# Performance work log

Hardware: AMD Instinct MI355X
Metric: run time of the kernel (lower is better)

Reference implementation:

```python
import jax, jax.numpy as jnp
import numpy as np

N_NODES = 50000
N_EDGES = 800000
MAX_ITER = 20  # torchdeq default f_max_iter=40; fixed iteration count for a tractable jit-able baseline
K = 3          # TAGConv default number of hops
INS, EMB, HID, OUT = 4, 64, 128, 1


def setup_inputs():
    key = jax.random.key(0)
    ks = jax.random.split(key, 12)
    def lin(k, fan_in, fan_out):
        return jax.random.normal(k, (fan_in, fan_out), jnp.float32) / np.sqrt(fan_in)
    def tag_w(k, fan_in, fan_out):
        # stacked weights for the K+1 TAGConv linear maps: [K+1, in, out]
        return jax.random.normal(k, (K + 1, fan_in, fan_out), jnp.float32) / np.sqrt(fan_in * (K + 1))
    return {
        "x": jax.random.normal(ks[0], (N_NODES, INS), jnp.float32),
        "pos": jax.random.normal(ks[1], (N_NODES, 3), jnp.float32),
        "edge_attr": jax.random.uniform(ks[2], (N_EDGES,), jnp.float32),
        "up_w1": lin(ks[3], INS, EMB), "up_b1": jnp.zeros((EMB,), jnp.float32),
        "up_w2": lin(ks[4], EMB, EMB), "up_b2": jnp.zeros((EMB,), jnp.float32),
        "c1_w": tag_w(ks[5], EMB + 3, HID), "c1_b": jnp.zeros((HID,), jnp.float32),
        "c2_w": tag_w(ks[6], HID, HID), "c2_b": jnp.zeros((HID,), jnp.float32),
        "c3_w": tag_w(ks[7], HID, EMB), "c3_b": jnp.zeros((EMB,), jnp.float32),
        "down_w1": lin(ks[8], EMB, OUT), "down_b1": jnp.zeros((OUT,), jnp.float32),
        "down_w2": lin(ks[9], OUT, OUT), "down_b2": jnp.zeros((OUT,), jnp.float32),
        "edge_index": jax.random.randint(ks[10], (2, N_EDGES), 0, N_NODES, jnp.int32),
    }


def _gcn_norm(row, col, edge_attr, n):
    # PyG gcn_norm with edge weights, no self loops (TAGConv default)
    deg = jax.ops.segment_sum(edge_attr, col, num_segments=n)
    safe = jnp.where(deg > 0, deg, 1.0)
    dinv = jnp.where(deg > 0, jax.lax.rsqrt(safe), 0.0)
    return dinv[row] * edge_attr * dinv[col]


def _mlp(x, w1, b1, w2, b2):
    # torch F.gelu default = exact erf gelu
    return jax.nn.gelu(x @ w1 + b1, approximate=False) @ w2 + b2


def reference(x, pos, edge_attr, up_w1, up_b1, up_w2, up_b2, c1_w, c1_b, c2_w, c2_b, c3_w, c3_b, down_w1, down_b1, down_w2, down_b2, edge_index):
    n = x.shape[0]
    row, col = edge_index[0], edge_index[1]
    norm = _gcn_norm(row, col, edge_attr, n)

    def tag(h, W, b):
        # TAGConv: sum_k lin_k( A_hat^k x ) + bias
        out = h @ W[0]
        for k in range(1, W.shape[0]):
            h = jax.ops.segment_sum(h[row] * norm[:, None], col, num_segments=n)  # [E,C] gather-scatter
            out = out + h @ W[k]
        return out + b

    def gnn(z):
        h = jnp.concatenate([z, pos], axis=1)
        h = jax.nn.relu(tag(h, c1_w, c1_b))
        h = jax.nn.relu(tag(h, c2_w, c2_b))  # F.dropout is identity in eval mode
        h = tag(h, c3_w, c3_b)
        return jax.nn.log_softmax(h, axis=1)

    z0 = _mlp(x, up_w1, up_b1, up_w2, up_b2)
    z = jax.lax.fori_loop(0, MAX_ITER, lambda i, zz: gnn(zz), z0)  # fixed-point solver
    z_star = gnn(z)  # phantom-gradient step (torchdeq grad=1)
    out = _mlp(z_star, down_w1, down_b1, down_w2, down_b2)
    return out, z_star
```

## Files before the change

### kernel.cpp

```cpp
#include <hip/hip_runtime.h>
#include <hip/hip_bf16.h>

#define N_NODES 50000
#define N_EDGES 800000
#define MAX_ITER 20

typedef __attribute__((ext_vector_type(8))) short bf16x8;
typedef __attribute__((ext_vector_type(4))) float f32x4;
typedef __attribute__((ext_vector_type(2))) float f32x2;
typedef unsigned char uchar;

__device__ __forceinline__ float gelu_f(float x){
  return 0.5f*x*(1.0f+erff(x*0.70710678118654752f));
}
__device__ __forceinline__ ushort f2b(float f){
  uint x = __float_as_uint(f);
  uint r = (x + 0x7fffu + ((x>>16)&1u)) >> 16;
  return (ushort)r;
}

#if __has_builtin(__builtin_amdgcn_cvt_pk_f32_fp8) && __has_builtin(__builtin_amdgcn_cvt_pk_fp8_f32)
#define HW_FP8 1
#endif

__device__ __forceinline__ uint fp8_enc1_sw(float x){
  uint u = __float_as_uint(x);
  uint s = (u>>24)&0x80u;
  int e = (int)((u>>23)&0xffu);
  uint m = u&0x7fffffu;
  uint m3 = (m + 0x80000u)>>20;
  if (m3==8u){ e+=1; m3=0u; }
  int e8 = e-120;
  if (e8<=0) return s;
  if (e8>=15) return s|0x7eu;
  return s | ((uint)e8<<3) | m3;
}
__device__ __forceinline__ float fp8_dec1_sw(uint b){
  uint s=(b&0x80u)<<24;
  uint em=b&0x7fu;
  if (em==0u) return __uint_as_float(s);
  if ((em>>3)==0u) return (s?-1.f:1.f)*(float)em*0.001953125f;
  return __uint_as_float(s | ((em+960u)<<20));
}
__device__ __forceinline__ void fp8_dec8(uint lo, uint hi, float* d){
#ifdef HW_FP8
  f32x2 a = __builtin_amdgcn_cvt_pk_f32_fp8(lo,false);
  f32x2 b = __builtin_amdgcn_cvt_pk_f32_fp8(lo,true);
  f32x2 c = __builtin_amdgcn_cvt_pk_f32_fp8(hi,false);
  f32x2 e = __builtin_amdgcn_cvt_pk_f32_fp8(hi,true);
  d[0]=a[0];d[1]=a[1];d[2]=b[0];d[3]=b[1];d[4]=c[0];d[5]=c[1];d[6]=e[0];d[7]=e[1];
#else
  d[0]=fp8_dec1_sw(lo&0xffu);        d[1]=fp8_dec1_sw((lo>>8)&0xffu);
  d[2]=fp8_dec1_sw((lo>>16)&0xffu);  d[3]=fp8_dec1_sw(lo>>24);
  d[4]=fp8_dec1_sw(hi&0xffu);        d[5]=fp8_dec1_sw((hi>>8)&0xffu);
  d[6]=fp8_dec1_sw((hi>>16)&0xffu);  d[7]=fp8_dec1_sw(hi>>24);
#endif
}
__device__ __forceinline__ uint fp8_enc4(float a,float b,float c,float d){
#ifdef HW_FP8
  uint u = __builtin_amdgcn_cvt_pk_fp8_f32(a,b,0u,false);
  u = __builtin_amdgcn_cvt_pk_fp8_f32(c,d,u,true);
  return u;
#else
  return fp8_enc1_sw(a) | (fp8_enc1_sw(b)<<8) | (fp8_enc1_sw(c)<<16) | (fp8_enc1_sw(d)<<24);
#endif
}
__device__ __forceinline__ uchar fp8_enc1(float a){
#ifdef HW_FP8
  return (uchar)(__builtin_amdgcn_cvt_pk_fp8_f32(a,a,0u,false)&0xffu);
#else
  return (uchar)fp8_enc1_sw(a);
#endif
}

__global__ void deg_cnt_kernel(const int* __restrict__ col, const float* __restrict__ attr,
                               float* __restrict__ deg, int* __restrict__ cnt){
  int e = blockIdx.x*256 + threadIdx.x;
  if (e < N_EDGES){
    int c = col[e];
    atomicAdd(&deg[c], attr[e]);
    atomicAdd(&cnt[c], 1);
  }
}

__global__ void norm_kernel(const int* __restrict__ row, const int* __restrict__ col,
                            const float* __restrict__ attr, const float* __restrict__ deg,
                            float* __restrict__ nrm){
  int e = blockIdx.x*256 + threadIdx.x;
  if (e < N_EDGES){
    float dr = deg[row[e]], dc = deg[col[e]];
    float ir = dr > 0.f ? rsqrtf(dr) : 0.f;
    float ic = dc > 0.f ? rsqrtf(dc) : 0.f;
    nrm[e] = ir * attr[e] * ic;
  }
}

__global__ void scan_kernel(const int* __restrict__ cnt, int* __restrict__ starts,
                            int* __restrict__ cursor){
  __shared__ int buf[1024];
  __shared__ int carry;
  int tid = threadIdx.x;
  if (tid==0) carry = 0;
  __syncthreads();
  for (int base=0; base<N_NODES; base+=1024){
    int i = base+tid;
    int v = (i<N_NODES)? cnt[i] : 0;
    int cv = carry;
    buf[tid]=v;
    __syncthreads();
    for (int off=1; off<1024; off<<=1){
      int t = (tid>=off)? buf[tid-off] : 0;
      __syncthreads();
      buf[tid]+=t;
      __syncthreads();
    }
    int excl = buf[tid]-v+cv;
    if (i<N_NODES){ starts[i]=excl; cursor[i]=excl; }
    __syncthreads();
    if (tid==0) carry = cv + buf[1023];
    __syncthreads();
  }
  if (tid==0) starts[N_NODES] = carry;
}

__global__ void fill_kernel(const int* __restrict__ row, const int* __restrict__ col,
                            const float* __restrict__ nrm, int* __restrict__ cursor,
                            int* __restrict__ csr_row, float* __restrict__ csr_nrm){
  int e = blockIdx.x*256+threadIdx.x;
  if (e<N_EDGES){
    int c = col[e];
    int p = atomicAdd(&cursor[c],1);
    csr_row[p]=row[e];
    csr_nrm[p]=nrm[e];
  }
}

__global__ void pack_w1(const float* __restrict__ W, ushort* __restrict__ PB){
  int i = blockIdx.x*256+threadIdx.x;
  if (i < 4*8*128*8){
    int e = i&7; int n = (i>>3)&127; int kb = (i>>10)&7; int j = i>>13;
    int k = kb*8+e;
    PB[i] = f2b(W[((size_t)j*67 + k)*128 + n]);
  }
}
__global__ void pack_w2(const float* __restrict__ W, ushort* __restrict__ PB){
  int i = blockIdx.x*256+threadIdx.x;
  if (i < 4*16*128*8){
    int e = i&7; int n = (i>>3)&127; int kb = (i>>10)&15; int j = i>>14;
    int k = kb*8+e;
    PB[i] = f2b(W[((size_t)j*128 + k)*128 + n]);
  }
}
__global__ void pack_w3(const float* __restrict__ W, ushort* __restrict__ PB){
  int i = blockIdx.x*256+threadIdx.x;
  if (i < 16*256*8){
    int e = i&7; int n = (i>>3)&255; int kb = i>>11;
    int k = kb*8+e;
    PB[i] = f2b(W[(((size_t)(n>>6))*128 + k)*64 + (n&63)]);
  }
}

__global__ __launch_bounds__(256) void mlp_up_kernel(
    const float* __restrict__ x, const float* __restrict__ w1, const float* __restrict__ b1,
    const float* __restrict__ w2, const float* __restrict__ b2,
    ushort* __restrict__ z, uchar* __restrict__ z8){
  __shared__ float sw1[4*64];
  __shared__ float sw2[64*64];
  __shared__ float sb1[64], sb2[64];
  __shared__ float t1s[4][64];
  int tid = threadIdx.x;
  for (int i=tid;i<256;i+=256) sw1[i]=w1[i];
  for (int i=tid;i<4096;i+=256) sw2[i]=w2[i];
  if (tid<64){ sb1[tid]=b1[tid]; sb2[tid]=b2[tid]; }
  __syncthreads();
  int g = tid>>6;
  int c = tid&63;
  int node = blockIdx.x*4 + g;
  float acc = sb1[c];
  #pragma unroll
  for (int k=0;k<4;k++) acc += x[node*4+k]*sw1[k*64+c];
  t1s[g][c] = gelu_f(acc);
  __syncthreads();
  float acc2 = sb2[c];
  #pragma unroll 8
  for (int k=0;k<64;k++) acc2 += t1s[g][k]*sw2[k*64+c];
  z[(size_t)node*64+c] = f2b(acc2);
  z8[(size_t)node*64+c] = fp8_enc1(acc2);
}

template<int LDIN>
__global__ void posprop(const float* __restrict__ in, float* __restrict__ out,
                        const int* __restrict__ starts, const int* __restrict__ crow,
                        const float* __restrict__ cnrm){
  int v = blockIdx.x*256+threadIdx.x;
  if (v >= N_NODES) return;
  int s=starts[v], e=starts[v+1];
  float a0=0.f,a1=0.f,a2=0.f;
  for (int i=s;i<e;++i){
    int r=crow[i]; float nm=cnrm[i];
    a0 = fmaf(in[(size_t)r*LDIN+0], nm, a0);
    a1 = fmaf(in[(size_t)r*LDIN+1], nm, a1);
    a2 = fmaf(in[(size_t)r*LDIN+2], nm, a2);
  }
  float4 o = {a0,a1,a2,0.f};
  *(float4*)(out + (size_t)v*4) = o;
}

__global__ __launch_bounds__(256) void posbias_kernel(
    const float* __restrict__ pos, const float* __restrict__ P1,
    const float* __restrict__ P2, const float* __restrict__ P3,
    const float* __restrict__ c1w, const float* __restrict__ c1b,
    ushort* __restrict__ pb){
  __shared__ float sw[4][3][128];
  int tid=threadIdx.x;
  for (int i=tid; i<4*3*128; i+=256){
    int cc=i&127; int d=(i>>7)%3; int j=i/(3*128);
    sw[j][d][cc] = c1w[((size_t)j*67 + 64 + d)*128 + cc];
  }
  __syncthreads();
  int idx = blockIdx.x*256+tid;
  if (idx < N_NODES*128){
    int n = idx>>7, cc = idx&127;
    float a = c1b[cc];
    #pragma unroll
    for (int d=0;d<3;d++) a = fmaf(pos[(size_t)n*3+d], sw[0][d][cc], a);
    #pragma unroll
    for (int d=0;d<3;d++) a = fmaf(P1[(size_t)n*4+d], sw[1][d][cc], a);
    #pragma unroll
    for (int d=0;d<3;d++) a = fmaf(P2[(size_t)n*4+d], sw[2][d][cc], a);
    #pragma unroll
    for (int d=0;d<3;d++) a = fmaf(P3[(size_t)n*4+d], sw[3][d][cc], a);
    pb[idx]=f2b(a);
  }
}

template<int MODE, bool IN8, bool OUT8>
__global__ __launch_bounds__(256) void prop64k(
    const void* __restrict__ hin, ushort* __restrict__ obf,
    uchar* __restrict__ of8, float* __restrict__ of32,
    const ushort* __restrict__ adj, const float* __restrict__ bias,
    const int* __restrict__ starts, const int* __restrict__ crow,
    const float* __restrict__ cnrm){
  constexpr bool WBF = (MODE==0) || (MODE==2) || (MODE==1 && !OUT8);
  int wv = threadIdx.x >> 6;
  int v = blockIdx.x*4 + wv;
  int t = threadIdx.x & 63;
  int g = t >> 3;
  int c = t & 7;
  int s = starts[v], e = starts[v+1];
  float acc[8] = {0,0,0,0,0,0,0,0};
  for (int i=s; i<e; i+=64){
    int cnt = e - i; if (cnt > 64) cnt = 64;
    int r = 0; float nm = 0.f;
    if (t < cnt){ r = crow[i+t]; nm = cnrm[i+t]; }
    for (int jb=0; jb<cnt; jb+=8){
      int rr = __shfl(r, jb+g, 64);
      float nmj = __shfl(nm, jb+g, 64);
      float hv[8];
      if (IN8){
        uint2 d = *(const uint2*)((const uchar*)hin + (size_t)rr*64 + c*8);
        fp8_dec8(d.x, d.y, hv);
      } else {
        uint4 d = *(const uint4*)((const ushort*)hin + (size_t)rr*64 + c*8);
        const uint* dp = (const uint*)&d;
        #pragma unroll
        for (int q=0;q<4;q++){
          hv[2*q]   = __uint_as_float(dp[q]<<16);
          hv[2*q+1] = __uint_as_float(dp[q]&0xffff0000u);
        }
      }
      #pragma unroll
      for (int q=0;q<8;q++) acc[q] = fmaf(hv[q], nmj, acc[q]);
    }
  }
  #pragma unroll
  for (int q=0;q<8;q++){
    acc[q] += __shfl_xor(acc[q], 8, 64);
    acc[q] += __shfl_xor(acc[q], 16, 64);
    acc[q] += __shfl_xor(acc[q], 32, 64);
  }
  if (MODE==0 || MODE==1){
    if (g==0){
      float val[8];
      if (MODE==1){
        uint4 av = *(const uint4*)(adj + (size_t)v*64 + c*8);
        const uint* ap=(const uint*)&av;
        #pragma unroll
        for (int q=0;q<4;q++){
          val[2*q]   = acc[2*q]   + __uint_as_float(ap[q]<<16);
          val[2*q+1] = acc[2*q+1] + __uint_as_float(ap[q]&0xffff0000u);
        }
      } else {
        #pragma unroll
        for (int q=0;q<8;q++) val[q]=acc[q];
      }
      if (WBF){
        uint4 o; uint* op=(uint*)&o;
        #pragma unroll
        for (int q=0;q<4;q++) op[q] = (uint)f2b(val[2*q]) | ((uint)f2b(val[2*q+1])<<16);
        *(uint4*)(obf + (size_t)v*64 + c*8) = o;
      }
      if (OUT8){
        uint2 o8;
        o8.x = fp8_enc4(val[0],val[1],val[2],val[3]);
        o8.y = fp8_enc4(val[4],val[5],val[6],val[7]);
        *(uint2*)(of8 + (size_t)v*64 + c*8) = o8;
      }
    }
  } else {
    uint4 av = *(const uint4*)(adj + (size_t)v*64 + c*8);
    const uint* ap=(const uint*)&av;
    float vv[8];
    #pragma unroll
    for (int q=0;q<4;q++){
      vv[2*q]   = acc[2*q]   + __uint_as_float(ap[q]<<16)         + bias[c*8+2*q];
      vv[2*q+1] = acc[2*q+1] + __uint_as_float(ap[q]&0xffff0000u) + bias[c*8+2*q+1];
    }
    float m = vv[0];
    #pragma unroll
    for (int q=1;q<8;q++) m = fmaxf(m, vv[q]);
    m = fmaxf(m, __shfl_xor(m,1,64));
    m = fmaxf(m, __shfl_xor(m,2,64));
    m = fmaxf(m, __shfl_xor(m,4,64));
    float ss = 0.f;
    #pragma unroll
    for (int q=0;q<8;q++) ss += __expf(vv[q]-m);
    ss += __shfl_xor(ss,1,64);
    ss += __shfl_xor(ss,2,64);
    ss += __shfl_xor(ss,4,64);
    float lse = m + __logf(ss);
    if (g==0){
      if (MODE==2){
        uint4 o; uint* op=(uint*)&o;
        #pragma unroll
        for (int q=0;q<4;q++) op[q] = (uint)f2b(vv[2*q]-lse) | ((uint)f2b(vv[2*q+1]-lse)<<16);
        *(uint4*)(obf + (size_t)v*64 + c*8) = o;
        if (OUT8){
          uint2 o8;
          o8.x = fp8_enc4(vv[0]-lse,vv[1]-lse,vv[2]-lse,vv[3]-lse);
          o8.y = fp8_enc4(vv[4]-lse,vv[5]-lse,vv[6]-lse,vv[7]-lse);
          *(uint2*)(of8 + (size_t)v*64 + c*8) = o8;
        }
      } else {
        float* zo = of32 + (size_t)v*64 + c*8;
        float4 o0 = {vv[0]-lse, vv[1]-lse, vv[2]-lse, vv[3]-lse};
        float4 o1 = {vv[4]-lse, vv[5]-lse, vv[6]-lse, vv[7]-lse};
        *(float4*)zo = o0;
        *(float4*)(zo+4) = o1;
      }
    }
  }
}

template<bool IN8, bool OUT8>
__global__ __launch_bounds__(256) void prop128k(
    const void* __restrict__ hin, ushort* __restrict__ obf,
    uchar* __restrict__ of8,
    const int* __restrict__ starts, const int* __restrict__ crow,
    const float* __restrict__ cnrm){
  int wv = threadIdx.x >> 6;
  int v = blockIdx.x*4 + wv;
  int t = threadIdx.x & 63;
  int g = t >> 4;
  int c = t & 15;
  int s = starts[v], e = starts[v+1];
  float acc[8] = {0,0,0,0,0,0,0,0};
  for (int i=s; i<e; i+=64){
    int cnt = e - i; if (cnt > 64) cnt = 64;
    int r = 0; float nm = 0.f;
    if (t < cnt){ r = crow[i+t]; nm = cnrm[i+t]; }
    for (int jb=0; jb<cnt; jb+=4){
      int rr  = __shfl(r,  jb+g, 64);
      float nmj = __shfl(nm, jb+g, 64);
      float hv[8];
      if (IN8){
        uint2 d = *(const uint2*)((const uchar*)hin + (size_t)rr*128 + c*8);
        fp8_dec8(d.x, d.y, hv);
      } else {
        uint4 d = *(const uint4*)((const ushort*)hin + (size_t)rr*128 + c*8);
        const uint* dp = (const uint*)&d;
        #pragma unroll
        for (int q=0;q<4;q++){
          hv[2*q]   = __uint_as_float(dp[q]<<16);
          hv[2*q+1] = __uint_as_float(dp[q]&0xffff0000u);
        }
      }
      #pragma unroll
      for (int q=0;q<8;q++) acc[q] = fmaf(hv[q], nmj, acc[q]);
    }
  }
  #pragma unroll
  for (int q=0;q<8;q++){
    acc[q] += __shfl_xor(acc[q], 16, 64);
    acc[q] += __shfl_xor(acc[q], 32, 64);
  }
  if (g==0){
    uint4 o; uint* op=(uint*)&o;
    #pragma unroll
    for (int q=0;q<4;q++) op[q] = (uint)f2b(acc[2*q]) | ((uint)f2b(acc[2*q+1])<<16);
    *(uint4*)(obf + (size_t)v*128 + c*8) = o;
    if (OUT8){
      uint2 o8;
      o8.x = fp8_enc4(acc[0],acc[1],acc[2],acc[3]);
      o8.y = fp8_enc4(acc[4],acc[5],acc[6],acc[7]);
      *(uint2*)(of8 + (size_t)v*128 + c*8) = o8;
    }
  }
}

template<int KC, bool PERNODE_BIAS, bool OUT8>
__global__ __launch_bounds__(256) void gemm4in(
    const ushort* __restrict__ H0, const ushort* __restrict__ H1,
    const ushort* __restrict__ H2, const ushort* __restrict__ H3,
    const ushort* __restrict__ PB, const void* __restrict__ biasp,
    ushort* __restrict__ out, uchar* __restrict__ out8){
  constexpr int NT = 8;
  constexpr int NKS = KC/32;
  int lane = threadIdx.x & 63;
  int wv   = threadIdx.x >> 6;
  int m0 = blockIdx.x*64 + wv*16;
  int lr = lane & 15, lg = lane >> 4;
  int arow = m0 + lr; if (arow > N_NODES-1) arow = N_NODES-1;
  const ushort* Hs[4] = {H0,H1,H2,H3};
  f32x4 acc[NT];
  #pragma unroll
  for (int t=0;t<NT;t++) acc[t] = (f32x4){0.f,0.f,0.f,0.f};
  #pragma unroll
  for (int j=0;j<4;j++){
    const ushort* Hj  = Hs[j] + (size_t)arow*KC + lg*8;
    const ushort* PBj = PB + (size_t)j*(KC/8)*128*8;
    #pragma unroll
    for (int ks=0; ks<NKS; ks++){
      bf16x8 af = *(const bf16x8*)(Hj + ks*32);
      int kb = ks*4 + lg;
      #pragma unroll
      for (int t=0;t<NT;t++){
        bf16x8 bf = *(const bf16x8*)(PBj + ((size_t)kb*128 + t*16 + lr)*8);
        acc[t] = __builtin_amdgcn_mfma_f32_16x16x32_bf16(af, bf, acc[t], 0, 0, 0);
      }
    }
  }
  #pragma unroll
  for (int t=0;t<NT;t++){
    #pragma unroll
    for (int q=0;q<4;q++){
      int node = m0 + lg*4 + q;
      if (node < N_NODES){
        int col = t*16 + lr;
        float b;
        if (PERNODE_BIAS) b = __uint_as_float(((uint)((const ushort*)biasp)[(size_t)node*128+col])<<16);
        else              b = ((const float*)biasp)[col];
        float vo = fmaxf(acc[t][q] + b, 0.f);
        out[(size_t)node*128 + col] = f2b(vo);
        if (OUT8) out8[(size_t)node*128 + col] = fp8_enc1(vo);
      }
    }
  }
}

__global__ __launch_bounds__(256) void gemm_y(
    const ushort* __restrict__ T2, const ushort* __restrict__ PB,
    ushort* __restrict__ Y, uchar* __restrict__ Y3_8){
  constexpr int NT = 16;
  int lane = threadIdx.x & 63;
  int wv   = threadIdx.x >> 6;
  int m0 = blockIdx.x*64 + wv*16;
  int lr = lane & 15, lg = lane >> 4;
  int arow = m0 + lr; if (arow > N_NODES-1) arow = N_NODES-1;
  f32x4 acc[NT];
  #pragma unroll
  for (int t=0;t<NT;t++) acc[t] = (f32x4){0.f,0.f,0.f,0.f};
  const ushort* Hj = T2 + (size_t)arow*128 + lg*8;
  #pragma unroll
  for (int ks=0; ks<4; ks++){
    bf16x8 af = *(const bf16x8*)(Hj + ks*32);
    int kb = ks*4 + lg;
    #pragma unroll
    for (int t=0;t<NT;t++){
      bf16x8 bf = *(const bf16x8*)(PB + ((size_t)kb*256 + t*16 + lr)*8);
      acc[t] = __builtin_amdgcn_mfma_f32_16x16x32_bf16(af, bf, acc[t], 0, 0, 0);
    }
  }
  #pragma unroll
  for (int t=0;t<NT;t++){
    int n = t*16 + lr;
    int j = n >> 6, cc = n & 63;
    #pragma unroll
    for (int q=0;q<4;q++){
      int node = m0 + lg*4 + q;
      if (node < N_NODES){
        Y[(size_t)j*N_NODES*64 + (size_t)node*64 + cc] = f2b(acc[t][q]);
        if (j==3) Y3_8[(size_t)node*64 + cc] = fp8_enc1(acc[t][q]);
      }
    }
  }
}

__global__ __launch_bounds__(256) void mlp_down_kernel(
    const float* __restrict__ zs, const float* __restrict__ dw1, const float* __restrict__ db1,
    const float* __restrict__ dw2, const float* __restrict__ db2, float* __restrict__ out){
  int node = blockIdx.x*4 + (threadIdx.x>>6);
  int c = threadIdx.x & 63;
  float v = zs[(size_t)node*64+c]*dw1[c];
  #pragma unroll
  for (int off=32; off; off>>=1) v += __shfl_xor(v, off, 64);
  if (c==0) out[node] = gelu_f(v + db1[0]) * dw2[0] + db2[0];
}

extern "C" void kernel_launch(void* const* d_in, const int* in_sizes, int n_in,
                              void* d_out, int out_size, void* d_ws, size_t ws_size,
                              hipStream_t stream){
  const float* x     = (const float*)d_in[0];
  const float* pos   = (const float*)d_in[1];
  const float* eattr = (const float*)d_in[2];
  const float* up_w1 = (const float*)d_in[3];
  const float* up_b1 = (const float*)d_in[4];
  const float* up_w2 = (const float*)d_in[5];
  const float* up_b2 = (const float*)d_in[6];
  const float* c1_w  = (const float*)d_in[7];
  const float* c1_b  = (const float*)d_in[8];
  const float* c2_w  = (const float*)d_in[9];
  const float* c2_b  = (const float*)d_in[10];
  const float* c3_w  = (const float*)d_in[11];
  const float* c3_b  = (const float*)d_in[12];
  const float* dw1   = (const float*)d_in[13];
  const float* db1   = (const float*)d_in[14];
  const float* dw2   = (const float*)d_in[15];
  const float* db2   = (const float*)d_in[16];
  const int*   eidx  = (const int*)d_in[17];
  const int* row = eidx;
  const int* col = eidx + N_EDGES;

  char* wsp = (char*)d_ws;
  size_t off = 0;
  auto alloc = [&](size_t bytes)->char*{
    char* p = wsp + off;
    off = (off + bytes + 255) & ~(size_t)255;
    return p;
  };
  float*  deg    = (float*)alloc((size_t)N_NODES*4);
  int*    cnt    = (int*)  alloc((size_t)N_NODES*4);
  int*    starts = (int*)  alloc((size_t)(N_NODES+1)*4);
  int*    cursor = (int*)  alloc((size_t)N_NODES*4);
  float*  nrm    = (float*)alloc((size_t)N_EDGES*4);
  int*    crow   = (int*)  alloc((size_t)N_EDGES*4);
  float*  cnrm   = (float*)alloc((size_t)N_EDGES*4);
  float*  P1     = (float*)alloc((size_t)N_NODES*4*4);
  float*  P2     = (float*)alloc((size_t)N_NODES*4*4);
  float*  P3     = (float*)alloc((size_t)N_NODES*4*4);
  ushort* pbias  = (ushort*)alloc((size_t)N_NODES*128*2);
  ushort* z      = (ushort*)alloc((size_t)N_NODES*64*2);
  ushort* q1     = (ushort*)alloc((size_t)N_NODES*64*2);
  ushort* q2     = (ushort*)alloc((size_t)N_NODES*64*2);
  ushort* q3     = (ushort*)alloc((size_t)N_NODES*64*2);
  ushort* t1     = (ushort*)alloc((size_t)N_NODES*128*2);
  ushort* p1     = (ushort*)alloc((size_t)N_NODES*128*2);
  ushort* p2     = (ushort*)alloc((size_t)N_NODES*128*2);
  ushort* p3     = (ushort*)alloc((size_t)N_NODES*128*2);
  ushort* t2     = (ushort*)alloc((size_t)N_NODES*128*2);
  ushort* PB1    = (ushort*)alloc((size_t)4*8*128*8*2);
  ushort* PB2    = (ushort*)alloc((size_t)4*16*128*8*2);
  ushort* PB3    = (ushort*)alloc((size_t)16*256*8*2);
  uchar*  z8     = (uchar*)alloc((size_t)N_NODES*64);
  uchar*  q1_8   = (uchar*)alloc((size_t)N_NODES*64);
  uchar*  q2_8   = (uchar*)alloc((size_t)N_NODES*64);
  uchar*  t1_8   = (uchar*)alloc((size_t)N_NODES*128);
  uchar*  p1_8   = (uchar*)alloc((size_t)N_NODES*128);
  uchar*  p2_8   = (uchar*)alloc((size_t)N_NODES*128);
  uchar*  Y3_8   = (uchar*)alloc((size_t)N_NODES*64);
  uchar*  u1_8   = (uchar*)alloc((size_t)N_NODES*64);
  uchar*  u2_8   = (uchar*)alloc((size_t)N_NODES*64);

  ushort* Y  = p1;
  ushort* Y0 = Y;
  ushort* Y1 = Y + (size_t)1*N_NODES*64;
  ushort* Y2 = Y + (size_t)2*N_NODES*64;
  ushort* Y3 = Y + (size_t)3*N_NODES*64;
  ushort* u1 = q1;
  ushort* u2 = q2;

  float* outv  = (float*)d_out;
  float* zstar = (float*)d_out + N_NODES;

  hipMemsetAsync(deg, 0, (size_t)N_NODES*4, stream);
  hipMemsetAsync(cnt, 0, (size_t)N_NODES*4, stream);
  int eb = (N_EDGES+255)/256;
  deg_cnt_kernel<<<eb,256,0,stream>>>(col, eattr, deg, cnt);
  norm_kernel<<<eb,256,0,stream>>>(row, col, eattr, deg, nrm);
  scan_kernel<<<1,1024,0,stream>>>(cnt, starts, cursor);
  fill_kernel<<<eb,256,0,stream>>>(row, col, nrm, cursor, crow, cnrm);
  pack_w1<<<128,256,0,stream>>>(c1_w, PB1);
  pack_w2<<<256,256,0,stream>>>(c2_w, PB2);
  pack_w3<<<128,256,0,stream>>>(c3_w, PB3);
  mlp_up_kernel<<<N_NODES/4,256,0,stream>>>(x, up_w1, up_b1, up_w2, up_b2, z, z8);

  int nb = (N_NODES+255)/256;
  posprop<3><<<nb,256,0,stream>>>(pos, P1, starts, crow, cnrm);
  posprop<4><<<nb,256,0,stream>>>(P1,  P2, starts, crow, cnrm);
  posprop<4><<<nb,256,0,stream>>>(P2,  P3, starts, crow, cnrm);
  posbias_kernel<<<(N_NODES*128)/256,256,0,stream>>>(pos, P1, P2, P3, c1_w, c1_b, pbias);

  const int gprop = N_NODES/4;
  const int ggemm = (N_NODES+63)/64;

  for (int it=0; it<=MAX_ITER; ++it){
    if (it < MAX_ITER){
      prop64k<0,true,true> <<<gprop,256,0,stream>>>(z8,   q1, q1_8, nullptr, nullptr, nullptr, starts, crow, cnrm);
      prop64k<0,true,true> <<<gprop,256,0,stream>>>(q1_8, q2, q2_8, nullptr, nullptr, nullptr, starts, crow, cnrm);
      prop64k<0,true,false><<<gprop,256,0,stream>>>(q2_8, q3, nullptr, nullptr, nullptr, nullptr, starts, crow, cnrm);
      gemm4in<64,true,true><<<ggemm,256,0,stream>>>(z,q1,q2,q3,PB1,pbias,t1,t1_8);

      prop128k<true,true> <<<gprop,256,0,stream>>>(t1_8, p1, p1_8, starts, crow, cnrm);
      prop128k<true,true> <<<gprop,256,0,stream>>>(p1_8, p2, p2_8, starts, crow, cnrm);
      prop128k<true,false><<<gprop,256,0,stream>>>(p2_8, p3, nullptr, starts, crow, cnrm);
      gemm4in<128,false,false><<<ggemm,256,0,stream>>>(t1,p1,p2,p3,PB2,c2_b,t2,nullptr);

      gemm_y<<<ggemm,256,0,stream>>>(t2, PB3, Y, Y3_8);
      prop64k<1,true,true><<<gprop,256,0,stream>>>(Y3_8, nullptr, u1_8, nullptr, Y2, nullptr, starts, crow, cnrm);
      prop64k<1,true,true><<<gprop,256,0,stream>>>(u1_8, nullptr, u2_8, nullptr, Y1, nullptr, starts, crow, cnrm);
      prop64k<2,true,true><<<gprop,256,0,stream>>>(u2_8, z, z8, nullptr, Y0, c3_b, starts, crow, cnrm);
    } else {
      prop64k<0,false,false><<<gprop,256,0,stream>>>(z,  q1, nullptr, nullptr, nullptr, nullptr, starts, crow, cnrm);
      prop64k<0,false,false><<<gprop,256,0,stream>>>(q1, q2, nullptr, nullptr, nullptr, nullptr, starts, crow, cnrm);
      prop64k<0,false,false><<<gprop,256,0,stream>>>(q2, q3, nullptr, nullptr, nullptr, nullptr, starts, crow, cnrm);
      gemm4in<64,true,false><<<ggemm,256,0,stream>>>(z,q1,q2,q3,PB1,pbias,t1,nullptr);

      prop128k<false,false><<<gprop,256,0,stream>>>(t1, p1, nullptr, starts, crow, cnrm);
      prop128k<false,false><<<gprop,256,0,stream>>>(p1, p2, nullptr, starts, crow, cnrm);
      prop128k<false,false><<<gprop,256,0,stream>>>(p2, p3, nullptr, starts, crow, cnrm);
      gemm4in<128,false,false><<<ggemm,256,0,stream>>>(t1,p1,p2,p3,PB2,c2_b,t2,nullptr);

      gemm_y<<<ggemm,256,0,stream>>>(t2, PB3, Y, Y3_8);
      prop64k<1,false,false><<<gprop,256,0,stream>>>(Y3, u1, nullptr, nullptr, Y2, nullptr, starts, crow, cnrm);
      prop64k<1,false,false><<<gprop,256,0,stream>>>(u1, u2, nullptr, nullptr, Y1, nullptr, starts, crow, cnrm);
      prop64k<3,false,false><<<gprop,256,0,stream>>>(u2, nullptr, nullptr, zstar, Y0, c3_b, starts, crow, cnrm);
    }
  }
  mlp_down_kernel<<<N_NODES/4,256,0,stream>>>(zstar, dw1, db1, dw2, db2, outv);
}
```

Before: 6.940 ms.

## Split 128-channel fp8 propagation into two 64-channel halves for cache locality

Stores the fp8 copies of 128-wide hidden features as two separate 64-byte-per-node planes and adds a propagation kernel in which each block gathers only one half. Block indices are interleaved so neighbouring blocks alternate halves, which shrinks the working set each gather touches and is meant to raise L2/MALL hit rates on the random edge gathers. In exchange every edge index and norm is read twice, the per-node reduction needs an extra shuffle stage, and twice as many blocks are launched.

```diff
diff --git a/kernel.cpp b/kernel.cpp
--- a/kernel.cpp
+++ b/kernel.cpp
@@ -352,10 +352,60 @@
   }
 }
 
-template<bool IN8, bool OUT8>
+template<bool OUT8>
+__global__ __launch_bounds__(256) void prop128s(
+    const uchar* __restrict__ inlo, const uchar* __restrict__ inhi,
+    ushort* __restrict__ obf, uchar* __restrict__ o8lo, uchar* __restrict__ o8hi,
+    const int* __restrict__ starts, const int* __restrict__ crow,
+    const float* __restrict__ cnrm){
+  int xs   = blockIdx.x & 7;
+  int half = xs >> 2;
+  int sub  = (blockIdx.x >> 3)*4 + (xs & 3);
+  const uchar* hin = half ? inhi : inlo;
+  uchar* of8 = half ? o8hi : o8lo;
+  int wv = threadIdx.x >> 6;
+  int v = sub*4 + wv;
+  int t = threadIdx.x & 63;
+  int g = t >> 3;
+  int c = t & 7;
+  int s = starts[v], e = starts[v+1];
+  float acc[8] = {0,0,0,0,0,0,0,0};
+  for (int i=s; i<e; i+=64){
+    int cnt = e - i; if (cnt > 64) cnt = 64;
+    int r = 0; float nm = 0.f;
+    if (t < cnt){ r = crow[i+t]; nm = cnrm[i+t]; }
+    for (int jb=0; jb<cnt; jb+=8){
+      int rr = __shfl(r, jb+g, 64);
+      float nmj = __shfl(nm, jb+g, 64);
+      float hv[8];
+      uint2 d = *(const uint2*)(hin + (size_t)rr*64 + c*8);
+      fp8_dec8(d.x, d.y, hv);
+      #pragma unroll
+      for (int q=0;q<8;q++) acc[q] = fmaf(hv[q], nmj, acc[q]);
+    }
+  }
+  #pragma unroll
+  for (int q=0;q<8;q++){
+    acc[q] += __shfl_xor(acc[q], 8, 64);
+    acc[q] += __shfl_xor(acc[q], 16, 64);
+    acc[q] += __shfl_xor(acc[q], 32, 64);
+  }
+  if (g==0){
+    uint4 o; uint* op=(uint*)&o;
+    #pragma unroll
+    for (int q=0;q<4;q++) op[q] = (uint)f2b(acc[2*q]) | ((uint)f2b(acc[2*q+1])<<16);
+    *(uint4*)(obf + (size_t)v*128 + half*64 + c*8) = o;
+    if (OUT8){
+      uint2 o8;
+      o8.x = fp8_enc4(acc[0],acc[1],acc[2],acc[3]);
+      o8.y = fp8_enc4(acc[4],acc[5],acc[6],acc[7]);
+      *(uint2*)(of8 + (size_t)v*64 + c*8) = o8;
+    }
+  }
+}
+
 __global__ __launch_bounds__(256) void prop128k(
-    const void* __restrict__ hin, ushort* __restrict__ obf,
-    uchar* __restrict__ of8,
+    const ushort* __restrict__ hin, ushort* __restrict__ obf,
     const int* __restrict__ starts, const int* __restrict__ crow,
     const float* __restrict__ cnrm){
   int wv = threadIdx.x >> 6;
@@ -372,21 +422,13 @@
     for (int jb=0; jb<cnt; jb+=4){
       int rr  = __shfl(r,  jb+g, 64);
       float nmj = __shfl(nm, jb+g, 64);
-      float hv[8];
-      if (IN8){
-        uint2 d = *(const uint2*)((const uchar*)hin + (size_t)rr*128 + c*8);
-        fp8_dec8(d.x, d.y, hv);
-      } else {
-        uint4 d = *(const uint4*)((const ushort*)hin + (size_t)rr*128 + c*8);
-        const uint* dp = (const uint*)&d;
-        #pragma unroll
-        for (int q=0;q<4;q++){
-          hv[2*q]   = __uint_as_float(dp[q]<<16);
-          hv[2*q+1] = __uint_as_float(dp[q]&0xffff0000u);
-        }
-      }
+      uint4 d = *(const uint4*)(hin + (size_t)rr*128 + c*8);
+      const uint* dp = (const uint*)&d;
       #pragma unroll
-      for (int q=0;q<8;q++) acc[q] = fmaf(hv[q], nmj, acc[q]);
+      for (int q=0;q<4;q++){
+        acc[2*q]   = fmaf(__uint_as_float(dp[q]<<16),         nmj, acc[2*q]);
+        acc[2*q+1] = fmaf(__uint_as_float(dp[q]&0xffff0000u), nmj, acc[2*q+1]);
+      }
     }
   }
   #pragma unroll
@@ -399,12 +441,6 @@
     #pragma unroll
     for (int q=0;q<4;q++) op[q] = (uint)f2b(acc[2*q]) | ((uint)f2b(acc[2*q+1])<<16);
     *(uint4*)(obf + (size_t)v*128 + c*8) = o;
-    if (OUT8){
-      uint2 o8;
-      o8.x = fp8_enc4(acc[0],acc[1],acc[2],acc[3]);
-      o8.y = fp8_enc4(acc[4],acc[5],acc[6],acc[7]);
-      *(uint2*)(of8 + (size_t)v*128 + c*8) = o8;
-    }
   }
 }
 
@@ -413,7 +449,7 @@
     const ushort* __restrict__ H0, const ushort* __restrict__ H1,
     const ushort* __restrict__ H2, const ushort* __restrict__ H3,
     const ushort* __restrict__ PB, const void* __restrict__ biasp,
-    ushort* __restrict__ out, uchar* __restrict__ out8){
+    ushort* __restrict__ out, uchar* __restrict__ out8lo, uchar* __restrict__ out8hi){
   constexpr int NT = 8;
   constexpr int NKS = KC/32;
   int lane = threadIdx.x & 63;
@@ -452,7 +488,10 @@
         else              b = ((const float*)biasp)[col];
         float vo = fmaxf(acc[t][q] + b, 0.f);
         out[(size_t)node*128 + col] = f2b(vo);
-        if (OUT8) out8[(size_t)node*128 + col] = fp8_enc1(vo);
+        if (OUT8){
+          if (col < 64) out8lo[(size_t)node*64 + col]      = fp8_enc1(vo);
+          else          out8hi[(size_t)node*64 + col - 64] = fp8_enc1(vo);
+        }
       }
     }
   }
@@ -564,9 +603,12 @@
   uchar*  z8     = (uchar*)alloc((size_t)N_NODES*64);
   uchar*  q1_8   = (uchar*)alloc((size_t)N_NODES*64);
   uchar*  q2_8   = (uchar*)alloc((size_t)N_NODES*64);
-  uchar*  t1_8   = (uchar*)alloc((size_t)N_NODES*128);
-  uchar*  p1_8   = (uchar*)alloc((size_t)N_NODES*128);
-  uchar*  p2_8   = (uchar*)alloc((size_t)N_NODES*128);
+  uchar*  t1_8lo = (uchar*)alloc((size_t)N_NODES*64);
+  uchar*  t1_8hi = (uchar*)alloc((size_t)N_NODES*64);
+  uchar*  p1_8lo = (uchar*)alloc((size_t)N_NODES*64);
+  uchar*  p1_8hi = (uchar*)alloc((size_t)N_NODES*64);
+  uchar*  p2_8lo = (uchar*)alloc((size_t)N_NODES*64);
+  uchar*  p2_8hi = (uchar*)alloc((size_t)N_NODES*64);
   uchar*  Y3_8   = (uchar*)alloc((size_t)N_NODES*64);
   uchar*  u1_8   = (uchar*)alloc((size_t)N_NODES*64);
   uchar*  u2_8   = (uchar*)alloc((size_t)N_NODES*64);
@@ -600,20 +642,21 @@
   posprop<4><<<nb,256,0,stream>>>(P2,  P3, starts, crow, cnrm);
   posbias_kernel<<<(N_NODES*128)/256,256,0,stream>>>(pos, P1, P2, P3, c1_w, c1_b, pbias);
 
-  const int gprop = N_NODES/4;
-  const int ggemm = (N_NODES+63)/64;
+  const int gprop  = N_NODES/4;
+  const int gsplit = N_NODES/2;
+  const int ggemm  = (N_NODES+63)/64;
 
   for (int it=0; it<=MAX_ITER; ++it){
     if (it < MAX_ITER){
       prop64k<0,true,true> <<<gprop,256,0,stream>>>(z8,   q1, q1_8, nullptr, nullptr, nullptr, starts, crow, cnrm);
       prop64k<0,true,true> <<<gprop,256,0,stream>>>(q1_8, q2, q2_8, nullptr, nullptr, nullptr, starts, crow, cnrm);
       prop64k<0,true,false><<<gprop,256,0,stream>>>(q2_8, q3, nullptr, nullptr, nullptr, nullptr, starts, crow, cnrm);
-      gemm4in<64,true,true><<<ggemm,256,0,stream>>>(z,q1,q2,q3,PB1,pbias,t1,t1_8);
-
-      prop128k<true,true> <<<gprop,256,0,stream>>>(t1_8, p1, p1_8, starts, crow, cnrm);
-      prop128k<true,true> <<<gprop,256,0,stream>>>(p1_8, p2, p2_8, starts, crow, cnrm);
-      prop128k<true,false><<<gprop,256,0,stream>>>(p2_8, p3, nullptr, starts, crow, cnrm);
-      gemm4in<128,false,false><<<ggemm,256,0,stream>>>(t1,p1,p2,p3,PB2,c2_b,t2,nullptr);
+      gemm4in<64,true,true><<<ggemm,256,0,stream>>>(z,q1,q2,q3,PB1,pbias,t1,t1_8lo,t1_8hi);
+
+      prop128s<true> <<<gsplit,256,0,stream>>>(t1_8lo,t1_8hi, p1, p1_8lo,p1_8hi, starts, crow, cnrm);
+      prop128s<true> <<<gsplit,256,0,stream>>>(p1_8lo,p1_8hi, p2, p2_8lo,p2_8hi, starts, crow, cnrm);
+      prop128s<false><<<gsplit,256,0,stream>>>(p2_8lo,p2_8hi, p3, nullptr,nullptr, starts, crow, cnrm);
+      gemm4in<128,false,false><<<ggemm,256,0,stream>>>(t1,p1,p2,p3,PB2,c2_b,t2,nullptr,nullptr);
 
       gemm_y<<<ggemm,256,0,stream>>>(t2, PB3, Y, Y3_8);
       prop64k<1,true,true><<<gprop,256,0,stream>>>(Y3_8, nullptr, u1_8, nullptr, Y2, nullptr, starts, crow, cnrm);
@@ -623,12 +666,12 @@
       prop64k<0,false,false><<<gprop,256,0,stream>>>(z,  q1, nullptr, nullptr, nullptr, nullptr, starts, crow, cnrm);
       prop64k<0,false,false><<<gprop,256,0,stream>>>(q1, q2, nullptr, nullptr, nullptr, nullptr, starts, crow, cnrm);
       prop64k<0,false,false><<<gprop,256,0,stream>>>(q2, q3, nullptr, nullptr, nullptr, nullptr, starts, crow, cnrm);
-      gemm4in<64,true,false><<<ggemm,256,0,stream>>>(z,q1,q2,q3,PB1,pbias,t1,nullptr);
-
-      prop128k<false,false><<<gprop,256,0,stream>>>(t1, p1, nullptr, starts, crow, cnrm);
-      prop128k<false,false><<<gprop,256,0,stream>>>(p1, p2, nullptr, starts, crow, cnrm);
-      prop128k<false,false><<<gprop,256,0,stream>>>(p2, p3, nullptr, starts, crow, cnrm);
-      gemm4in<128,false,false><<<ggemm,256,0,stream>>>(t1,p1,p2,p3,PB2,c2_b,t2,nullptr);
+      gemm4in<64,true,false><<<ggemm,256,0,stream>>>(z,q1,q2,q3,PB1,pbias,t1,nullptr,nullptr);
+
+      prop128k<<<gprop,256,0,stream>>>(t1, p1, starts, crow, cnrm);
+      prop128k<<<gprop,256,0,stream>>>(p1, p2, starts, crow, cnrm);
+      prop128k<<<gprop,256,0,stream>>>(p2, p3, starts, crow, cnrm);
+      gemm4in<128,false,false><<<ggemm,256,0,stream>>>(t1,p1,p2,p3,PB2,c2_b,t2,nullptr,nullptr);
 
       gemm_y<<<ggemm,256,0,stream>>>(t2, PB3, Y, Y3_8);
       prop64k<1,false,false><<<gprop,256,0,stream>>>(Y3, u1, nullptr, nullptr, Y2, nullptr, starts, crow, cnrm);
```

Result: slower. 7.664 ms (+10.4%).
